# Kernel optimization log

Measured on AMD Instinct MI355X. Metric: run time of the kernel, lower is better.

The kernel has to match this reference:

```python
import jax, jax.numpy as jnp
import numpy as np
from jax import lax

EPS = 1e-3  # Keras LayerNormalization default epsilon

def _layernorm(x, g, b):
    m = jnp.mean(x, axis=-1, keepdims=True)
    v = jnp.var(x, axis=-1, keepdims=True)
    return (x - m) * lax.rsqrt(v + EPS) * g + b

def _conv1d_same(x, w, b, stride):
    # x: (B, T, Cin), w: (K, Cin, Cout) -> (B, ceil(T/stride), Cout), TF 'same' padding
    y = lax.conv_general_dilated(x, w, window_strides=(stride,), padding='SAME',
                                 dimension_numbers=('NWC', 'WIO', 'NWC'))
    return y + b

def _process(x, conv1_w, conv1_b, ln1_g, ln1_b, conv2_w, conv2_b, ln2_g, ln2_b):
    # SmallConvNet (dropout omitted for deterministic reference)
    x = _conv1d_same(x, conv1_w, conv1_b, 3)
    x = jax.nn.silu(_layernorm(x, ln1_g, ln1_b))
    x = _conv1d_same(x, conv2_w, conv2_b, 5)
    x = jax.nn.silu(_layernorm(x, ln2_g, ln2_b))
    return x

def setup_inputs() -> dict:
    key = jax.random.key(0)
    ks = jax.random.split(key, 4)
    B, T, E = 4, 1920, 512
    return {
        'values':  jax.random.normal(ks[0], (B, T, E), jnp.float32),
        'symbols': jax.random.normal(ks[1], (T, E), jnp.float32),
        'conv1_w': jax.random.normal(ks[2], (5, E, 128), jnp.float32) * 0.05,
        'conv1_b': jnp.zeros((128,), jnp.float32),
        'ln1_g':   jnp.ones((128,), jnp.float32),
        'ln1_b':   jnp.zeros((128,), jnp.float32),
        'conv2_w': jax.random.normal(ks[3], (3, 128, 1024), jnp.float32) * 0.05,
        'conv2_b': jnp.zeros((1024,), jnp.float32),
        'ln2_g':   jnp.ones((1024,), jnp.float32),
        'ln2_b':   jnp.zeros((1024,), jnp.float32),
    }

def reference(values, symbols, conv1_w, conv1_b, ln1_g, ln1_b, conv2_w, conv2_b, ln2_g, ln2_b):
    proc = lambda x: _process(x, conv1_w, conv1_b, ln1_g, ln1_b, conv2_w, conv2_b, ln2_g, ln2_b)
    values_projected = proc(values)                                     # (B, n, d)
    symbol_projected = proc(jnp.broadcast_to(symbols, values.shape))    # (B, n, d)
    # symbolic=True: sign-cosine similarity of X_i vs (X_i + C_j)
    a = values_projected[:, None, :, :]                                 # (B, 1, n, d) -> i on axis 2
    b = a + symbol_projected[:, :, None, :]                             # (B, n, n, d) -> j on axis 1
    S = jnp.mean(jnp.sign(a) * jnp.sign(b), axis=-1)                    # (B, n, n)
    scores = jax.nn.softmax(S, axis=-1)
    attention_output = jnp.einsum('bji,bid->bjd', scores, values_projected)
    O = jax.nn.silu(attention_output * symbol_projected)
    return (O, values_projected)
```

## Files before the change

### kernel.cpp

```cpp
#include <hip/hip_runtime.h>
#include <math.h>

#define LN_EPS 1e-3f

typedef __attribute__((ext_vector_type(8))) short short8;
typedef __attribute__((ext_vector_type(4))) float floatx4;

__device__ __forceinline__ float silu_f(float x) { return x / (1.f + expf(-x)); }

__device__ __forceinline__ int mism1(float a, float s) {
    unsigned ua = __float_as_uint(a);
    unsigned ub = __float_as_uint(a + s);
    return (int)((ua ^ ub) >> 31);
}

__device__ __forceinline__ short f2bf(float f) {
    unsigned u = __float_as_uint(f);
    unsigned r = (u + 0x7FFFu + ((u >> 16) & 1u)) >> 16;
    return (short)r;
}

__global__ __launch_bounds__(256) void k_prep(
    const float* __restrict__ w1,
    const float* __restrict__ w2,
    short* __restrict__ w1s,
    short* __restrict__ w2s)
{
    int tid = blockIdx.x * 256 + threadIdx.x;
    if (tid < 327680) {
        int j    = tid & 7;
        int lane = (tid >> 3) & 63;
        int nt   = (tid >> 9) & 7;
        int ks   = (tid >> 12) % 10;
        int kc   = tid / 40960;
        int kw = ks >> 1;
        int ci = kc * 64 + (ks & 1) * 32 + ((lane >> 4) & 3) * 8 + j;
        int n  = nt * 16 + (lane & 15);
        w1s[tid] = f2bf(w1[((size_t)(kw * 512 + ci)) * 128 + n]);
    } else {
        int t = tid - 327680;
        if (t < 393216) {
            int j    = t & 7;
            int lane = (t >> 3) & 63;
            int nt   = (t >> 9) & 63;
            int ks   = t >> 15;
            int k  = ks * 32 + ((lane >> 4) & 3) * 8 + j;
            int kw = k >> 7;
            int ci = k & 127;
            int n  = nt * 16 + (lane & 15);
            w2s[t] = f2bf(w2[((size_t)(kw * 128 + ci)) * 1024 + n]);
        }
    }
}

__global__ __launch_bounds__(512) void k_conv1m(
    const float* __restrict__ values,
    const float* __restrict__ symbols,
    const short* __restrict__ w1s,
    const float* __restrict__ b1,
    const float* __restrict__ g1,
    const float* __restrict__ bt1,
    short* __restrict__ h1)
{
    int mt  = blockIdx.x;
    int seq = mt / 40;
    int tl  = mt % 40;
    const float* x = (seq < 4) ? (values + (size_t)seq * 1920 * 512) : symbols;
    int p0 = 48 * tl - 1;

    __shared__ short xs[50 * 520];
    __shared__ float red[8][4][4][2];

    int tid  = threadIdx.x;
    int lane = tid & 63, w = tid >> 6;
    int quad = lane >> 4, mrow = lane & 15;

    for (int idx = tid; idx < 6400; idx += 512) {
        int r = idx >> 7, g = idx & 127;
        int gp = p0 + r;
        float4 v = make_float4(0.f, 0.f, 0.f, 0.f);
        if (gp >= 0 && gp < 1920)
            v = *(const float4*)(x + (size_t)gp * 512 + 4 * g);
        short4 pk;
        pk.x = f2bf(v.x); pk.y = f2bf(v.y); pk.z = f2bf(v.z); pk.w = f2bf(v.w);
        *(short4*)(xs + r * 520 + 4 * g) = pk;
    }
    __syncthreads();

    floatx4 acc = (floatx4){0.f, 0.f, 0.f, 0.f};
    for (int kc = 0; kc < 8; kc++) {
        #pragma unroll
        for (int ks = 0; ks < 10; ks++) {
            int kw  = ks >> 1;
            int ci  = kc * 64 + (ks & 1) * 32 + quad * 8;
            short8 a = *(const short8*)(xs + (3 * mrow + kw) * 520 + ci);
            short8 b = *(const short8*)(w1s +
                (((size_t)(kc * 10 + ks) * 8 + w) * 64 + lane) * 8);
            acc = __builtin_amdgcn_mfma_f32_16x16x32_bf16(a, b, acc, 0, 0, 0);
        }
    }

    int co = w * 16 + mrow;
    float b1v = b1[co], g1v = g1[co], btv = bt1[co];

    float s1[4], s2[4];
    #pragma unroll
    for (int r = 0; r < 4; r++) {
        float v = acc[r] + b1v;
        acc[r] = v;
        s1[r] = v; s2[r] = v * v;
    }
    #pragma unroll
    for (int m = 8; m >= 1; m >>= 1) {
        #pragma unroll
        for (int r = 0; r < 4; r++) {
            s1[r] += __shfl_xor(s1[r], m, 64);
            s2[r] += __shfl_xor(s2[r], m, 64);
        }
    }
    if (mrow == 0) {
        #pragma unroll
        for (int r = 0; r < 4; r++) { red[w][quad][r][0] = s1[r]; red[w][quad][r][1] = s2[r]; }
    }
    __syncthreads();

    #pragma unroll
    for (int r = 0; r < 4; r++) {
        float S1 = 0.f, S2 = 0.f;
        #pragma unroll
        for (int ww = 0; ww < 8; ww++) { S1 += red[ww][quad][r][0]; S2 += red[ww][quad][r][1]; }
        float mean = S1 * (1.f / 128.f);
        float var  = S2 * (1.f / 128.f) - mean * mean;
        float rs   = rsqrtf(var + LN_EPS);
        int row = seq * 640 + tl * 16 + quad * 4 + r;
        float o = silu_f((acc[r] - mean) * rs * g1v + btv);
        h1[(size_t)row * 128 + co] = f2bf(o);
    }
}

__global__ __launch_bounds__(1024) void k_conv2m(
    const short* __restrict__ h1,
    const short* __restrict__ w2s,
    const float* __restrict__ b2,
    const float* __restrict__ g2,
    const float* __restrict__ bt2,
    float* __restrict__ vp,
    float* __restrict__ sp)
{
    int blk  = blockIdx.x;
    int pos0 = blk * 16;
    int seq  = pos0 >> 7;
    int lcl0 = pos0 & 127;
    int row0 = seq * 640 + 5 * lcl0;

    __shared__ short xa[78 * 136];
    __shared__ float red[16][4][4][2];

    int tid = threadIdx.x;
    int lane = tid & 63, w = tid >> 6;
    int quad = lane >> 4, mrow = lane & 15;

    for (int idx = tid; idx < 78 * 16; idx += 1024) {
        int r = idx >> 4, g = idx & 15;
        *(short8*)(xa + r * 136 + g * 8) =
            *(const short8*)(h1 + (size_t)(row0 + r) * 128 + g * 8);
    }
    __syncthreads();

    floatx4 acc[4];
    #pragma unroll
    for (int nt = 0; nt < 4; nt++) acc[nt] = (floatx4){0.f, 0.f, 0.f, 0.f};

    #pragma unroll
    for (int ks = 0; ks < 12; ks++) {
        int kw  = ks >> 2;
        int ci0 = (ks & 3) * 32;
        short8 a = *(const short8*)(xa + (5 * mrow + kw) * 136 + ci0 + quad * 8);
        #pragma unroll
        for (int nt = 0; nt < 4; nt++) {
            short8 b = *(const short8*)(w2s +
                (((size_t)ks * 64 + w * 4 + nt) * 64 + lane) * 8);
            acc[nt] = __builtin_amdgcn_mfma_f32_16x16x32_bf16(a, b, acc[nt], 0, 0, 0);
        }
    }

    float b2v[4], g2v[4], btv[4];
    #pragma unroll
    for (int nt = 0; nt < 4; nt++) {
        int co = w * 64 + nt * 16 + mrow;
        b2v[nt] = b2[co]; g2v[nt] = g2[co]; btv[nt] = bt2[co];
    }

    float s1[4] = {0.f, 0.f, 0.f, 0.f}, s2[4] = {0.f, 0.f, 0.f, 0.f};
    #pragma unroll
    for (int nt = 0; nt < 4; nt++)
        #pragma unroll
        for (int r = 0; r < 4; r++) {
            float v = acc[nt][r] + b2v[nt];
            acc[nt][r] = v;
            s1[r] += v; s2[r] += v * v;
        }
    #pragma unroll
    for (int m = 8; m >= 1; m >>= 1) {
        #pragma unroll
        for (int r = 0; r < 4; r++) {
            s1[r] += __shfl_xor(s1[r], m, 64);
            s2[r] += __shfl_xor(s2[r], m, 64);
        }
    }
    if (mrow == 0) {
        #pragma unroll
        for (int r = 0; r < 4; r++) { red[w][quad][r][0] = s1[r]; red[w][quad][r][1] = s2[r]; }
    }
    __syncthreads();

    float mean[4], rs[4];
    #pragma unroll
    for (int r = 0; r < 4; r++) {
        float S1 = 0.f, S2 = 0.f;
        #pragma unroll
        for (int ww = 0; ww < 16; ww++) { S1 += red[ww][quad][r][0]; S2 += red[ww][quad][r][1]; }
        mean[r] = S1 * (1.f / 1024.f);
        float var = S2 * (1.f / 1024.f) - mean[r] * mean[r];
        rs[r] = rsqrtf(var + LN_EPS);
    }

    float* obase = (pos0 < 512) ? (vp + (size_t)pos0 * 1024)
                                : (sp + (size_t)(pos0 - 512) * 1024);
    #pragma unroll
    for (int nt = 0; nt < 4; nt++) {
        int co = w * 64 + nt * 16 + mrow;
        #pragma unroll
        for (int r = 0; r < 4; r++) {
            float o = silu_f((acc[nt][r] - mean[r]) * rs[r] * g2v[nt] + btv[nt]);
            obase[((size_t)(quad * 4 + r)) * 1024 + co] = o;
        }
    }
}

__global__ __launch_bounds__(1024) void k_attn(
    const float* __restrict__ vp,
    const float* __restrict__ sp,
    float* __restrict__ O)
{
    int b  = blockIdx.x >> 6;
    int j0 = (blockIdx.x & 63) * 2;
    int tid = threadIdx.x, lane = tid & 63, wv = tid >> 6;

    __shared__ float  ss[2][1024];
    __shared__ int    cc[8][128][2];
    __shared__ float  sc0[128], sc1[128];
    __shared__ float  reds[2][16];
    __shared__ float4 redc[4][2][256];

    if (tid < 512) {
        int jj = tid >> 8, g = tid & 255;
        *(float4*)(&ss[jj][4 * g]) = *(const float4*)(sp + (size_t)(j0 + jj) * 1024 + 4 * g);
    }
    __syncthreads();

    {
        int i = tid >> 3, sub = tid & 7;
        const float* vrow = vp + ((size_t)(b * 128 + i)) * 1024;
        int m0 = 0, m1 = 0;
        #pragma unroll 8
        for (int k = 0; k < 32; k++) {
            int q = 4 * (sub + 8 * k);
            float4 v  = *(const float4*)(vrow + q);
            float4 s0 = *(const float4*)(&ss[0][q]);
            float4 s1 = *(const float4*)(&ss[1][q]);
            m0 += mism1(v.x, s0.x) + mism1(v.y, s0.y) + mism1(v.z, s0.z) + mism1(v.w, s0.w);
            m1 += mism1(v.x, s1.x) + mism1(v.y, s1.y) + mism1(v.z, s1.z) + mism1(v.w, s1.w);
        }
        cc[sub][i][0] = m0;
        cc[sub][i][1] = m1;
    }
    __syncthreads();

    float e0 = 0.f, e1 = 0.f;
    if (tid < 128) {
        int c0 = 0, c1 = 0;
        #pragma unroll
        for (int s = 0; s < 8; s++) { c0 += cc[s][tid][0]; c1 += cc[s][tid][1]; }
        e0 = expf(1.f - (float)c0 * (2.f / 1024.f));
        e1 = expf(1.f - (float)c1 * (2.f / 1024.f));
    }
    float t0 = e0, t1 = e1;
    #pragma unroll
    for (int m = 32; m >= 1; m >>= 1) {
        t0 += __shfl_xor(t0, m, 64);
        t1 += __shfl_xor(t1, m, 64);
    }
    if (lane == 0) { reds[0][wv] = t0; reds[1][wv] = t1; }
    __syncthreads();
    if (tid < 128) {
        float tot0 = 0.f, tot1 = 0.f;
        #pragma unroll
        for (int ww = 0; ww < 16; ww++) { tot0 += reds[0][ww]; tot1 += reds[1][ww]; }
        sc0[tid] = e0 / tot0;
        sc1[tid] = e1 / tot1;
    }
    __syncthreads();

    {
        int dloc = tid & 255, iq = tid >> 8;
        int dd = 4 * dloc;
        const float* vpb = vp + (size_t)b * 131072 + (size_t)iq * 32 * 1024;
        float4 a0 = make_float4(0.f, 0.f, 0.f, 0.f);
        float4 a1 = make_float4(0.f, 0.f, 0.f, 0.f);
        #pragma unroll 8
        for (int k = 0; k < 32; k++) {
            float4 v = *(const float4*)(vpb + (size_t)k * 1024 + dd);
            float f0 = sc0[iq * 32 + k];
            float f1 = sc1[iq * 32 + k];
            a0.x += f0 * v.x; a0.y += f0 * v.y; a0.z += f0 * v.z; a0.w += f0 * v.w;
            a1.x += f1 * v.x; a1.y += f1 * v.y; a1.z += f1 * v.z; a1.w += f1 * v.w;
        }
        redc[iq][0][dloc] = a0;
        redc[iq][1][dloc] = a1;
    }
    __syncthreads();
    if (tid < 512) {
        int jj = tid >> 8, dloc = tid & 255;
        int dd = 4 * dloc;
        float4 r0 = redc[0][jj][dloc], r1 = redc[1][jj][dloc];
        float4 r2 = redc[2][jj][dloc], r3 = redc[3][jj][dloc];
        float4 ao;
        ao.x = r0.x + r1.x + r2.x + r3.x;
        ao.y = r0.y + r1.y + r2.y + r3.y;
        ao.z = r0.z + r1.z + r2.z + r3.z;
        ao.w = r0.w + r1.w + r2.w + r3.w;
        float4 o;
        o.x = silu_f(ao.x * ss[jj][dd + 0]);
        o.y = silu_f(ao.y * ss[jj][dd + 1]);
        o.z = silu_f(ao.z * ss[jj][dd + 2]);
        o.w = silu_f(ao.w * ss[jj][dd + 3]);
        *(float4*)(O + ((size_t)(b * 128 + j0 + jj)) * 1024 + dd) = o;
    }
}

extern "C" void kernel_launch(void* const* d_in, const int* in_sizes, int n_in,
                              void* d_out, int out_size, void* d_ws, size_t ws_size,
                              hipStream_t stream) {
    const float* values  = (const float*)d_in[0];
    const float* symbols = (const float*)d_in[1];
    const float* conv1_w = (const float*)d_in[2];
    const float* conv1_b = (const float*)d_in[3];
    const float* ln1_g   = (const float*)d_in[4];
    const float* ln1_b   = (const float*)d_in[5];
    const float* conv2_w = (const float*)d_in[6];
    const float* conv2_b = (const float*)d_in[7];
    const float* ln2_g   = (const float*)d_in[8];
    const float* ln2_b   = (const float*)d_in[9];

    float* out = (float*)d_out;
    float* O   = out;
    float* vp  = out + 4 * 128 * 1024;

    float* sp  = (float*)d_ws;
    short* h1  = (short*)(sp + 128 * 1024);
    short* w1s = h1 + 3200 * 128;
    short* w2s = w1s + 327680;

    k_prep<<<2816, 256, 0, stream>>>(conv1_w, conv2_w, w1s, w2s);
    k_conv1m<<<200, 512, 0, stream>>>(values, symbols, w1s,
                                      conv1_b, ln1_g, ln1_b, h1);
    k_conv2m<<<40, 1024, 0, stream>>>(h1, w2s, conv2_b, ln2_g, ln2_b, vp, sp);
    k_attn<<<256, 1024, 0, stream>>>(vp, sp, O);
}
```

Measured before the change: 133.6 us.

## Split attention into tiled sign-count kernel and softmax-weighted sum kernel

The single attention kernel becomes two. k_count tiles over 16 j rows and 128-wide d chunks, keeps each thread's value row in registers and reuses it across 16 symbol rows, then writes partial mismatch counts to workspace. k_sein sums those partials, does the softmax, and computes the weighted sum for 8 j rows per block, so each vp load is reused 8 times instead of 2. This cuts repeated global reads of vp, at the cost of an extra launch and a round trip of partial counts through memory.

```diff
diff --git a/kernel.cpp b/kernel.cpp
--- a/kernel.cpp
+++ b/kernel.cpp
@@ -238,104 +238,129 @@
     }
 }
 
-__global__ __launch_bounds__(1024) void k_attn(
+__global__ __launch_bounds__(1024) void k_count(
     const float* __restrict__ vp,
     const float* __restrict__ sp,
+    int* __restrict__ S_part)
+{
+    int b  = blockIdx.x >> 6;
+    int jg = (blockIdx.x >> 3) & 7;
+    int dc = blockIdx.x & 7;
+    int tid = threadIdx.x;
+
+    __shared__ float sls[8 * 260];
+    __shared__ int   cnt[16][128];
+
+    if (tid < 512) {
+        int r = tid >> 5, c = tid & 31;
+        float4 v = *(const float4*)(sp + (size_t)(jg * 16 + r) * 1024 + dc * 128 + 4 * c);
+        int sub = c >> 2, off = (c & 3) * 4;
+        *(float4*)&sls[sub * 260 + r * 16 + off] = v;
+    }
+    __syncthreads();
+
+    int i = tid >> 3, sub = tid & 7;
+    const float* vr = vp + ((size_t)(b * 128 + i)) * 1024 + dc * 128 + sub * 16;
+    float4 v0 = *(const float4*)(vr + 0);
+    float4 v1 = *(const float4*)(vr + 4);
+    float4 v2 = *(const float4*)(vr + 8);
+    float4 v3 = *(const float4*)(vr + 12);
+
+    const float* sbase = &sls[sub * 260];
+    #pragma unroll
+    for (int j = 0; j < 16; j++) {
+        const float4* srow = (const float4*)(sbase + j * 16);
+        float4 s0 = srow[0], s1 = srow[1], s2 = srow[2], s3 = srow[3];
+        int m = mism1(v0.x, s0.x) + mism1(v0.y, s0.y) + mism1(v0.z, s0.z) + mism1(v0.w, s0.w)
+              + mism1(v1.x, s1.x) + mism1(v1.y, s1.y) + mism1(v1.z, s1.z) + mism1(v1.w, s1.w)
+              + mism1(v2.x, s2.x) + mism1(v2.y, s2.y) + mism1(v2.z, s2.z) + mism1(v2.w, s2.w)
+              + mism1(v3.x, s3.x) + mism1(v3.y, s3.y) + mism1(v3.z, s3.z) + mism1(v3.w, s3.w);
+        m += __shfl_xor(m, 1, 64);
+        m += __shfl_xor(m, 2, 64);
+        m += __shfl_xor(m, 4, 64);
+        if (sub == 0) cnt[j][i] = m;
+    }
+    __syncthreads();
+
+    #pragma unroll
+    for (int t = 0; t < 2; t++) {
+        int idx = tid + t * 1024;
+        int j = idx >> 7, ii = idx & 127;
+        S_part[(((size_t)(b * 128 + jg * 16 + j)) * 8 + dc) * 128 + ii] = cnt[j][ii];
+    }
+}
+
+__global__ __launch_bounds__(1024) void k_sein(
+    const float* __restrict__ vp,
+    const float* __restrict__ sp,
+    const int* __restrict__ S_part,
     float* __restrict__ O)
 {
     int b  = blockIdx.x >> 6;
-    int j0 = (blockIdx.x & 63) * 2;
-    int tid = threadIdx.x, lane = tid & 63, wv = tid >> 6;
-
-    __shared__ float  ss[2][1024];
-    __shared__ int    cc[8][128][2];
-    __shared__ float  sc0[128], sc1[128];
-    __shared__ float  reds[2][16];
-    __shared__ float4 redc[4][2][256];
+    int jo = (blockIdx.x >> 2) & 15;
+    int dq = blockIdx.x & 3;
+    int tid = threadIdx.x;
+
+    __shared__ float  sc[8][128];
+    __shared__ float4 pacc[8][8][64];
+    __shared__ float  reds[8][2];
+
+    {
+        int jj = tid >> 7, ii = tid & 127;
+        int j  = jo * 8 + jj;
+        const int* cb = S_part + ((size_t)(b * 128 + j)) * 8 * 128 + ii;
+        int c = 0;
+        #pragma unroll
+        for (int dcc = 0; dcc < 8; dcc++) c += cb[dcc * 128];
+        float e = expf(1.f - (float)c * (2.f / 1024.f));
+        float t = e;
+        #pragma unroll
+        for (int m = 32; m >= 1; m >>= 1) t += __shfl_xor(t, m, 64);
+        if ((tid & 63) == 0) reds[jj][(tid >> 6) & 1] = t;
+        __syncthreads();
+        float tot = reds[jj][0] + reds[jj][1];
+        sc[jj][ii] = e / tot;
+    }
+    __syncthreads();
 
     if (tid < 512) {
-        int jj = tid >> 8, g = tid & 255;
-        *(float4*)(&ss[jj][4 * g]) = *(const float4*)(sp + (size_t)(j0 + jj) * 1024 + 4 * g);
-    }
-    __syncthreads();
-
-    {
-        int i = tid >> 3, sub = tid & 7;
-        const float* vrow = vp + ((size_t)(b * 128 + i)) * 1024;
-        int m0 = 0, m1 = 0;
-        #pragma unroll 8
-        for (int k = 0; k < 32; k++) {
-            int q = 4 * (sub + 8 * k);
-            float4 v  = *(const float4*)(vrow + q);
-            float4 s0 = *(const float4*)(&ss[0][q]);
-            float4 s1 = *(const float4*)(&ss[1][q]);
-            m0 += mism1(v.x, s0.x) + mism1(v.y, s0.y) + mism1(v.z, s0.z) + mism1(v.w, s0.w);
-            m1 += mism1(v.x, s1.x) + mism1(v.y, s1.y) + mism1(v.z, s1.z) + mism1(v.w, s1.w);
-        }
-        cc[sub][i][0] = m0;
-        cc[sub][i][1] = m1;
-    }
-    __syncthreads();
-
-    float e0 = 0.f, e1 = 0.f;
-    if (tid < 128) {
-        int c0 = 0, c1 = 0;
-        #pragma unroll
-        for (int s = 0; s < 8; s++) { c0 += cc[s][tid][0]; c1 += cc[s][tid][1]; }
-        e0 = expf(1.f - (float)c0 * (2.f / 1024.f));
-        e1 = expf(1.f - (float)c1 * (2.f / 1024.f));
-    }
-    float t0 = e0, t1 = e1;
-    #pragma unroll
-    for (int m = 32; m >= 1; m >>= 1) {
-        t0 += __shfl_xor(t0, m, 64);
-        t1 += __shfl_xor(t1, m, 64);
-    }
-    if (lane == 0) { reds[0][wv] = t0; reds[1][wv] = t1; }
-    __syncthreads();
-    if (tid < 128) {
-        float tot0 = 0.f, tot1 = 0.f;
-        #pragma unroll
-        for (int ww = 0; ww < 16; ww++) { tot0 += reds[0][ww]; tot1 += reds[1][ww]; }
-        sc0[tid] = e0 / tot0;
-        sc1[tid] = e1 / tot1;
-    }
-    __syncthreads();
-
-    {
-        int dloc = tid & 255, iq = tid >> 8;
-        int dd = 4 * dloc;
-        const float* vpb = vp + (size_t)b * 131072 + (size_t)iq * 32 * 1024;
-        float4 a0 = make_float4(0.f, 0.f, 0.f, 0.f);
-        float4 a1 = make_float4(0.f, 0.f, 0.f, 0.f);
-        #pragma unroll 8
-        for (int k = 0; k < 32; k++) {
-            float4 v = *(const float4*)(vpb + (size_t)k * 1024 + dd);
-            float f0 = sc0[iq * 32 + k];
-            float f1 = sc1[iq * 32 + k];
-            a0.x += f0 * v.x; a0.y += f0 * v.y; a0.z += f0 * v.z; a0.w += f0 * v.w;
-            a1.x += f1 * v.x; a1.y += f1 * v.y; a1.z += f1 * v.z; a1.w += f1 * v.w;
-        }
-        redc[iq][0][dloc] = a0;
-        redc[iq][1][dloc] = a1;
-    }
-    __syncthreads();
+        int ig = tid >> 6, dcol = tid & 63;
+        const float* vb = vp + ((size_t)(b * 128 + ig * 16)) * 1024 + dq * 256 + 4 * dcol;
+        float4 acc[8];
+        #pragma unroll
+        for (int jj = 0; jj < 8; jj++) acc[jj] = make_float4(0.f, 0.f, 0.f, 0.f);
+        #pragma unroll 4
+        for (int k = 0; k < 16; k++) {
+            float4 v = *(const float4*)(vb + (size_t)k * 1024);
+            #pragma unroll
+            for (int jj = 0; jj < 8; jj++) {
+                float s = sc[jj][ig * 16 + k];
+                acc[jj].x += s * v.x; acc[jj].y += s * v.y;
+                acc[jj].z += s * v.z; acc[jj].w += s * v.w;
+            }
+        }
+        #pragma unroll
+        for (int jj = 0; jj < 8; jj++) pacc[ig][jj][dcol] = acc[jj];
+    }
+    __syncthreads();
+
     if (tid < 512) {
-        int jj = tid >> 8, dloc = tid & 255;
-        int dd = 4 * dloc;
-        float4 r0 = redc[0][jj][dloc], r1 = redc[1][jj][dloc];
-        float4 r2 = redc[2][jj][dloc], r3 = redc[3][jj][dloc];
-        float4 ao;
-        ao.x = r0.x + r1.x + r2.x + r3.x;
-        ao.y = r0.y + r1.y + r2.y + r3.y;
-        ao.z = r0.z + r1.z + r2.z + r3.z;
-        ao.w = r0.w + r1.w + r2.w + r3.w;
+        int jj = tid >> 6, dcol = tid & 63;
+        float4 a = pacc[0][jj][dcol];
+        #pragma unroll
+        for (int ig = 1; ig < 8; ig++) {
+            float4 p = pacc[ig][jj][dcol];
+            a.x += p.x; a.y += p.y; a.z += p.z; a.w += p.w;
+        }
+        int j = jo * 8 + jj;
+        int d = dq * 256 + 4 * dcol;
+        float4 sv = *(const float4*)(sp + (size_t)j * 1024 + d);
         float4 o;
-        o.x = silu_f(ao.x * ss[jj][dd + 0]);
-        o.y = silu_f(ao.y * ss[jj][dd + 1]);
-        o.z = silu_f(ao.z * ss[jj][dd + 2]);
-        o.w = silu_f(ao.w * ss[jj][dd + 3]);
-        *(float4*)(O + ((size_t)(b * 128 + j0 + jj)) * 1024 + dd) = o;
+        o.x = silu_f(a.x * sv.x);
+        o.y = silu_f(a.y * sv.y);
+        o.z = silu_f(a.z * sv.z);
+        o.w = silu_f(a.w * sv.w);
+        *(float4*)(O + ((size_t)(b * 128 + j)) * 1024 + d) = o;
     }
 }
 
@@ -361,10 +386,12 @@
     short* h1  = (short*)(sp + 128 * 1024);
     short* w1s = h1 + 3200 * 128;
     short* w2s = w1s + 327680;
+    int*   S_part = (int*)(w2s + 393216);
 
     k_prep<<<2816, 256, 0, stream>>>(conv1_w, conv2_w, w1s, w2s);
     k_conv1m<<<200, 512, 0, stream>>>(values, symbols, w1s,
                                       conv1_b, ln1_g, ln1_b, h1);
     k_conv2m<<<40, 1024, 0, stream>>>(h1, w2s, conv2_b, ln2_g, ln2_b, vp, sp);
-    k_attn<<<256, 1024, 0, stream>>>(vp, sp, O);
-}
+    k_count<<<256, 1024, 0, stream>>>(vp, sp, S_part);
+    k_sein<<<256, 1024, 0, stream>>>(vp, sp, S_part, O);
+}
```

Result: no change. 132.2 us (-1.1%).
